# Performance work log

Measured on AMD Instinct MI355X. Metric: run time of the kernel, lower is better.

The kernel has to match this reference:

```python
import jax, jax.numpy as jnp
from jax import lax
import numpy as np

N_QUBITS = 4
N_LAYERS = 2


def _apply_gate(state, M, w):
    # state: [B, 2,2,2,2]; M: [2,2] shared or [B,2,2] batched; acts on wire w
    s = jnp.moveaxis(state, w + 1, 1)
    if M.ndim == 3:
        s = jnp.einsum('bij,bj...->bi...', M, s)
    else:
        s = jnp.einsum('ij,bj...->bi...', M, s)
    return jnp.moveaxis(s, 1, w + 1)


def _apply_cnot(state, c, t):
    # c < t always (chain CNOTs). Move control axis to 1; target axis (t+1) unchanged.
    s = jnp.moveaxis(state, c + 1, 1)
    s0 = s[:, 0]
    s1 = jnp.flip(s[:, 1], axis=t)  # target axis after dropping axis1 is t+1-1 = t
    s = jnp.stack([s0, s1], axis=1)
    return jnp.moveaxis(s, 1, c + 1)


def _quantum_head(q_input, qparams):
    # q_input: [B, n_qubits] rotation angles; qparams: [n_layers, n_qubits, 3]
    B = q_input.shape[0]
    state = jnp.zeros((B, 2 ** N_QUBITS), jnp.complex64).at[:, 0].set(1.0)
    state = state.reshape((B,) + (2,) * N_QUBITS)
    # RY feature map (batched matrices)
    for i in range(N_QUBITS):
        th = q_input[:, i]
        c, s = jnp.cos(th / 2), jnp.sin(th / 2)
        M = jnp.stack([jnp.stack([c, -s], -1), jnp.stack([s, c], -1)], -2)  # [B,2,2]
        state = _apply_gate(state, M.astype(jnp.complex64), i)
    # variational layers
    for layer in range(N_LAYERS):
        for i in range(N_QUBITS):
            phi = qparams[layer, i, 0]
            th = qparams[layer, i, 1]
            om = qparams[layer, i, 2]
            c, s = jnp.cos(th / 2), jnp.sin(th / 2)
            hs, hd = 0.5 * (phi + om), 0.5 * (phi - om)
            M = jnp.stack([
                jnp.stack([jnp.exp(-1j * hs) * c, -jnp.exp(1j * hd) * s]),
                jnp.stack([jnp.exp(-1j * hd) * s, jnp.exp(1j * hs) * c]),
            ])  # [2,2] shared across batch (Rot = RZ(om) RY(th) RZ(phi))
            state = _apply_gate(state, M.astype(jnp.complex64), i)
        for i in range(N_QUBITS - 1):
            state = _apply_cnot(state, i, i + 1)
    # <Z_0> = P(q0=0) - P(q0=1)
    probs = state.real ** 2 + state.imag ** 2
    probs = probs.reshape(B, 2, -1)
    return probs[:, 0].sum(-1) - probs[:, 1].sum(-1)


def _maxpool21(x):
    return lax.reduce_window(x, -np.inf, lax.max, (1, 1, 2, 2), (1, 1, 1, 1), 'VALID')


def setup_inputs() -> dict:
    key = jax.random.key(0)
    ks = jax.random.split(key, 8)
    r = lambda k, s, sc: jax.random.normal(k, s, jnp.float32) * sc
    return {
        'inputs': jax.random.normal(ks[0], (128, 3, 250, 250), jnp.float32),
        'conv1_w': r(ks[1], (6, 3, 5, 5), 0.1),
        'conv1_b': jnp.zeros((6,), jnp.float32),
        'conv2_w': r(ks[2], (15, 6, 3, 3), 0.1),
        'conv2_b': jnp.zeros((15,), jnp.float32),
        'fc1_w': r(ks[3], (120, 55815), 0.004),
        'fc1_b': jnp.zeros((120,), jnp.float32),
        'fc2_w': r(ks[4], (84, 120), 0.09),
        'fc2_b': jnp.zeros((84,), jnp.float32),
        'fc3_w': r(ks[5], (1, 84), 0.1),
        'fc3_b': jnp.zeros((1,), jnp.float32),
        'qparams': jax.random.normal(ks[6], (N_LAYERS, N_QUBITS, 3), jnp.float32),
    }


def reference(inputs, conv1_w, conv1_b, conv2_w, conv2_b, fc1_w, fc1_b,
              fc2_w, fc2_b, fc3_w, fc3_b, qparams):
    dn = ('NCHW', 'OIHW', 'NCHW')
    x = lax.conv_general_dilated(inputs, conv1_w, (2, 2), [(1, 1), (1, 1)],
                                 dimension_numbers=dn) + conv1_b[None, :, None, None]
    x = _maxpool21(jax.nn.relu(x))          # [B,6,123,123]
    x = lax.conv_general_dilated(x, conv2_w, (2, 2), [(1, 1), (1, 1)],
                                 dimension_numbers=dn) + conv2_b[None, :, None, None]
    x = _maxpool21(jax.nn.relu(x))          # [B,15,61,61]
    x = x.reshape(x.shape[0], -1)           # [B,55815]
    x = jax.nn.relu(x @ fc1_w.T + fc1_b)
    x = jax.nn.relu(x @ fc2_w.T + fc2_b)
    x = (x @ fc3_w.T + fc3_b)[:, 0]         # [B]
    q_input = jnp.repeat(x[:, None], N_QUBITS, axis=1)
    q_out = _quantum_head(q_input, qparams)  # [B]
    probs = 0.5 * (q_out + 1.0)
    return jnp.stack([probs, 1.0 - probs], axis=-1)
```

## Files before the change

kernel.cpp:

```cpp
#include <hip/hip_runtime.h>

#define SPLITK 256
#define FC1_K 55815
#define KP 55816

__device__ __forceinline__ unsigned short f2bf(float f) {
    unsigned u = __float_as_uint(f);
    return (unsigned short)((u + 0x7FFFu + ((u >> 16) & 1u)) >> 16);
}

__global__ __launch_bounds__(256) void conv1f_k(const float* __restrict__ in,
                                                const float* __restrict__ w,
                                                const float* __restrict__ bias,
                                                float* __restrict__ out) {
    __shared__ float sbuf[4608];
    const int tc = blockIdx.x, tr = blockIdx.y, b = blockIdx.z;
    const int pr0 = tr * 31, pc0 = tc * 31;
    const int tid = threadIdx.x;
    const int i = tid >> 4, j = tid & 15;
    const int wv = tid >> 6;
    const float* inb = in + (size_t)b * 187500;
    const int ir0 = 2 * pr0 - 1, ic0 = 2 * pc0 - 1;

    {
        int y = tid / 68, x = tid - y * 68;
        #pragma unroll
        for (int it = 0; it < 18; ++it) {
            int gr = ir0 + y, gc = ic0 + x;
            if (!((unsigned)gr < 250u && (unsigned)gc < 250u))
                sbuf[tid + it * 256] = 0.0f;
            x += 52; y += 3;
            if (x >= 68) { x -= 68; ++y; }
        }
    }

    float acc[6][2][2];
    #pragma unroll
    for (int o = 0; o < 6; ++o) {
        float bv = bias[o];
        acc[o][0][0] = bv; acc[o][0][1] = bv; acc[o][1][0] = bv; acc[o][1][1] = bv;
    }

    auto compute_ch = [&](int c) {
        #pragma unroll
        for (int wr = 0; wr < 7; ++wr) {
            const float* rp = &sbuf[(4 * i + wr) * 68 + 4 * j];
            float row[7];
            float4 v4 = *(const float4*)rp;
            float2 v2 = *(const float2*)(rp + 4);
            row[0] = v4.x; row[1] = v4.y; row[2] = v4.z; row[3] = v4.w;
            row[4] = v2.x; row[5] = v2.y; row[6] = rp[6];
            #pragma unroll
            for (int o = 0; o < 6; ++o) {
                #pragma unroll
                for (int kw = 0; kw < 5; ++kw) {
                    if (wr <= 4) {
                        float wv_ = w[o * 75 + c * 25 + wr * 5 + kw];
                        acc[o][0][0] = fmaf(row[kw], wv_, acc[o][0][0]);
                        acc[o][0][1] = fmaf(row[kw + 2], wv_, acc[o][0][1]);
                    }
                    if (wr >= 2) {
                        float wv_ = w[o * 75 + c * 25 + (wr - 2) * 5 + kw];
                        acc[o][1][0] = fmaf(row[kw], wv_, acc[o][1][0]);
                        acc[o][1][1] = fmaf(row[kw + 2], wv_, acc[o][1][1]);
                    }
                }
            }
        }
    };

    for (int c = 0; c < 3; ++c) {
        __syncthreads();
        const float* cp = inb + c * 62500;
        {
            int y = tid / 68, x = tid - y * 68;
            #pragma unroll
            for (int it = 0; it < 18; ++it) {
                int gr = ir0 + y, gc = ic0 + x;
                if ((unsigned)gr < 250u && (unsigned)gc < 250u) {
                    const float* gp = cp + gr * 250 + gc;
                    __builtin_amdgcn_global_load_lds(
                        (const __attribute__((address_space(1))) void*)gp,
                        (__attribute__((address_space(3))) void*)&sbuf[it * 256 + wv * 64],
                        4, 0, 0);
                }
                x += 52; y += 3;
                if (x >= 68) { x -= 68; ++y; }
            }
        }
        __syncthreads();
        compute_ch(c);
    }
    __syncthreads();

    const int gr0 = pr0 + 2 * i, gc0 = pc0 + 2 * j;
    const bool r1in = (2 * i + 1 < 31) && (gr0 + 1 < 123);
    const bool c1in = (2 * j + 1 < 31) && (gc0 + 1 < 123);
    const bool r0in = gr0 < 123, c0in = gc0 < 123;
    #pragma unroll
    for (int g = 0; g < 2; ++g) {
        #pragma unroll
        for (int oo = 0; oo < 3; ++oo)
            #pragma unroll
            for (int di = 0; di < 2; ++di)
                #pragma unroll
                for (int dj = 0; dj < 2; ++dj)
                    sbuf[(oo * 32 + 2 * i + di) * 33 + (2 * j + dj)] =
                        fmaxf(acc[g * 3 + oo][di][dj], 0.0f);
        __syncthreads();
        #pragma unroll
        for (int oo = 0; oo < 3; ++oo) {
            int o = g * 3 + oo;
            const float* p0 = &sbuf[(oo * 32 + 2 * i) * 33 + 2 * j];
            float c00 = p0[0],  c01 = p0[1],  c02 = p0[2];
            float c10 = p0[33], c11 = p0[34], c12 = p0[35];
            float c20 = p0[66], c21 = p0[67], c22 = p0[68];
            float* orow = out + ((size_t)(b * 6 + o) * 123 + gr0) * 123 + gc0;
            if (r0in && c0in) orow[0]   = fmaxf(fmaxf(c00, c01), fmaxf(c10, c11));
            if (r0in && c1in) orow[1]   = fmaxf(fmaxf(c01, c02), fmaxf(c11, c12));
            if (r1in && c0in) orow[123] = fmaxf(fmaxf(c10, c11), fmaxf(c20, c21));
            if (r1in && c1in) orow[124] = fmaxf(fmaxf(c11, c12), fmaxf(c21, c22));
        }
        __syncthreads();
    }
}

__global__ __launch_bounds__(256) void conv2f_k(const float* __restrict__ in,
                                                const float* __restrict__ w,
                                                const float* __restrict__ bias,
                                                unsigned short* __restrict__ out) {
    __shared__ float smem[2000];
    const int tc = blockIdx.x, tr = blockIdx.y, b = blockIdx.z;
    const int pr0 = tr * 15, pc0 = tc * 15;
    const int tid = threadIdx.x;
    const int wv = tid >> 6, lane = tid & 63;
    const int ti = tid >> 4, tj = tid & 15;
    const int tl = ti & 3;
    float* wreg = smem + wv * 320;
    float* halo = smem + 1280;
    const float* inb = in + (size_t)b * 6 * 15129;
    const int irw = 2 * pr0 - 1 + 8 * wv;
    const int ic0 = 2 * pc0 - 1;
    const bool safe = (tr >= 1 && tr <= 3) && (tc >= 1 && tc <= 3);

    int off[5];
    unsigned msk = 0u;
    {
        int y = (lane >= 34) ? 1 : 0;
        int x = lane - 34 * y;
        #pragma unroll
        for (int it = 0; it < 5; ++it) {
            int gr = irw + y, gc = ic0 + x;
            bool valid = ((unsigned)gr < 123u) && ((unsigned)gc < 123u);
            off[it] = valid ? (gr * 123 + gc) : 0;
            msk |= (valid ? 1u : 0u) << it;
            x += 30; ++y;
            if (x >= 34) { x -= 34; ++y; }
        }
    }

    float acc[15];
    #pragma unroll
    for (int o = 0; o < 15; ++o) acc[o] = bias[o];

    for (int c = 0; c < 6; ++c) {
        const float* cp = inb + c * 15129;
        if (safe) {
            #pragma unroll
            for (int it = 0; it < 5; ++it) wreg[lane + it * 64] = cp[off[it]];
        } else {
            #pragma unroll
            for (int it = 0; it < 5; ++it) {
                float v = 0.0f;
                if ((msk >> it) & 1u) v = cp[off[it]];
                wreg[lane + it * 64] = v;
            }
        }
        #pragma unroll
        for (int kh = 0; kh < 3; ++kh) {
            const float* r = &wreg[(2 * tl + kh) * 34 + 2 * tj];
            float a0 = r[0], a1 = r[1], a2 = r[2];
            #pragma unroll
            for (int o = 0; o < 15; ++o) {
                const float* wr_ = &w[o * 54 + c * 9 + kh * 3];
                acc[o] = fmaf(a0, wr_[0], acc[o]);
                acc[o] = fmaf(a1, wr_[1], acc[o]);
                acc[o] = fmaf(a2, wr_[2], acc[o]);
            }
        }
    }

    if (tl == 0 && wv > 0) {
        #pragma unroll
        for (int o = 0; o < 15; ++o)
            halo[(wv - 1) * 240 + o * 16 + tj] = acc[o];
    }
    __syncthreads();

    const int gr = pr0 + ti, gc = pc0 + tj;
    const bool valid = (ti < 15) && (tj < 15) && (gr < 61) && (gc < 61);
    const bool lastrow = (tl == 3);
    const int hb = (wv < 2 ? wv : 2) * 240;
    #pragma unroll
    for (int o = 0; o < 15; ++o) {
        float c00 = acc[o];
        float c01 = __shfl(acc[o], lane + 1);
        float s10 = __shfl(acc[o], lane + 16);
        float s11 = __shfl(acc[o], lane + 17);
        float h10 = halo[hb + o * 16 + tj];
        float h11 = halo[hb + o * 16 + (tj + 1 > 15 ? 15 : tj + 1)];
        float c10 = lastrow ? h10 : s10;
        float c11 = lastrow ? h11 : s11;
        float m = fmaxf(fmaxf(fmaxf(c00, c01), fmaxf(c10, c11)), 0.0f);
        if (valid) out[(size_t)b * KP + o * 3721 + gr * 61 + gc] = f2bf(m);
    }
}

__global__ __launch_bounds__(256) void wcvt_k(const float* __restrict__ W,
                                              unsigned short* __restrict__ Wb) {
    const int n = blockIdx.y;
    const float* src = W + (size_t)n * FC1_K;
    unsigned int* dst = (unsigned int*)(Wb + (size_t)n * KP);
    int base = blockIdx.x * 2048 + threadIdx.x * 2;
    #pragma unroll
    for (int p = 0; p < 4; ++p) {
        int k2 = base + p * 512;
        if (k2 < FC1_K) {
            float v0 = src[k2];
            float v1 = (k2 + 1 < FC1_K) ? src[k2 + 1] : 0.0f;
            dst[k2 >> 1] = (unsigned)f2bf(v0) | ((unsigned)f2bf(v1) << 16);
        }
    }
}

__global__ __launch_bounds__(256) void fc1_k(const unsigned short* __restrict__ Xb,
                                             const unsigned short* __restrict__ Wb,
                                             float* __restrict__ P) {
    using short8 = __attribute__((ext_vector_type(8))) short;
    using f32x4 = __attribute__((ext_vector_type(4))) float;
    __shared__ unsigned short Xs[2][128][40];
    __shared__ unsigned short Ws[2][128][40];
    const int s = blockIdx.x;
    const int ks = s * 224;
    const int ke = min(ks + 224, FC1_K);
    const int tid = threadIdx.x;
    const int row = tid >> 1, cb = (tid & 1) * 16;
    const int wv = tid >> 6, lane = tid & 63;
    const int kb = lane >> 4, lr = lane & 15;

    f32x4 acc[2][8];
    #pragma unroll
    for (int mt = 0; mt < 2; ++mt)
        #pragma unroll
        for (int nt = 0; nt < 8; ++nt)
            acc[mt][nt] = (f32x4){0.f, 0.f, 0.f, 0.f};

    const int nsteps = (ke > ks) ? ((ke - ks + 31) >> 5) : 0;

    auto stage = [&](int buf, int st) {
        const int k0 = ks + st * 32;
        const int krem = ke - k0;
        const unsigned short* xsrc = Xb + (size_t)row * KP + k0 + cb;
        #pragma unroll
        for (int q = 0; q < 2; ++q) {
            int g = cb + q * 8;
            if (g + 8 <= krem) {
                *(uint4*)&Xs[buf][row][g] = *(const uint4*)(xsrc + q * 8);
            } else {
                #pragma unroll
                for (int jj = 0; jj < 8; ++jj)
                    Xs[buf][row][g + jj] = (g + jj < krem) ? xsrc[q * 8 + jj] : (unsigned short)0;
            }
        }
        if (row < 120) {
            const unsigned short* wsrc = Wb + (size_t)row * KP + k0 + cb;
            #pragma unroll
            for (int q = 0; q < 2; ++q) {
                int g = cb + q * 8;
                if (g + 8 <= krem) {
                    *(uint4*)&Ws[buf][row][g] = *(const uint4*)(wsrc + q * 8);
                } else {
                    #pragma unroll
                    for (int jj = 0; jj < 8; ++jj)
                        Ws[buf][row][g + jj] = (g + jj < krem) ? wsrc[q * 8 + jj] : (unsigned short)0;
                }
            }
        } else {
            uint4 z = {0u, 0u, 0u, 0u};
            *(uint4*)&Ws[buf][row][cb] = z;
            *(uint4*)&Ws[buf][row][cb + 8] = z;
        }
    };

    if (nsteps > 0) stage(0, 0);
    int cur = 0;
    for (int st = 0; st < nsteps; ++st) {
        __syncthreads();
        if (st + 1 < nsteps) stage(cur ^ 1, st + 1);
        short8 afr[2];
        #pragma unroll
        for (int mt = 0; mt < 2; ++mt)
            afr[mt] = *(const short8*)&Xs[cur][(wv * 2 + mt) * 16 + lr][kb * 8];
        #pragma unroll
        for (int nt = 0; nt < 8; ++nt) {
            short8 bfr = *(const short8*)&Ws[cur][nt * 16 + lr][kb * 8];
            #pragma unroll
            for (int mt = 0; mt < 2; ++mt)
                acc[mt][nt] = __builtin_amdgcn_mfma_f32_16x16x32_bf16(afr[mt], bfr, acc[mt][nt], 0, 0, 0);
        }
        cur ^= 1;
    }

    float* Pp = P + (size_t)s * 15360;
    #pragma unroll
    for (int mt = 0; mt < 2; ++mt)
        #pragma unroll
        for (int nt = 0; nt < 8; ++nt)
            #pragma unroll
            for (int r = 0; r < 4; ++r) {
                int m = (wv * 2 + mt) * 16 + kb * 4 + r;
                int n = nt * 16 + lr;
                if (n < 120) Pp[m * 120 + n] = acc[mt][nt][r];
            }
}

__global__ __launch_bounds__(512) void tail_k(const float* __restrict__ P,
                                              const float* __restrict__ f1b,
                                              const float* __restrict__ f2w,
                                              const float* __restrict__ f2b,
                                              const float* __restrict__ f3w,
                                              const float* __restrict__ f3b,
                                              const float* __restrict__ qp,
                                              float* __restrict__ out) {
    __shared__ float red[4][120];
    __shared__ float x1[120];
    __shared__ float x2[84];
    int b = blockIdx.x, tid = threadIdx.x;
    if (tid < 480) {
        int part = tid / 120;
        int n = tid - part * 120;
        const float* p = P + (size_t)b * 120 + n;
        float acc = 0.0f;
        #pragma unroll 8
        for (int s = part; s < SPLITK; s += 4)
            acc += p[(size_t)s * 15360];
        red[part][n] = acc;
    }
    __syncthreads();
    if (tid < 120)
        x1[tid] = fmaxf((red[0][tid] + red[1][tid]) + (red[2][tid] + red[3][tid]) + f1b[tid], 0.0f);
    __syncthreads();
    if (tid < 84) {
        float acc = f2b[tid];
        const float* wr = f2w + tid * 120;
        #pragma unroll 4
        for (int n = 0; n < 120; ++n) acc = fmaf(x1[n], wr[n], acc);
        x2[tid] = fmaxf(acc, 0.0f);
    }
    __syncthreads();
    if (tid == 0) {
        float x = f3b[0];
        for (int m = 0; m < 84; ++m) x = fmaf(x2[m], f3w[m], x);
        float sr[16], si[16];
        #pragma unroll
        for (int i = 0; i < 16; ++i) { sr[i] = 0.0f; si[i] = 0.0f; }
        sr[0] = 1.0f;
        float c0 = cosf(0.5f * x), s0 = sinf(0.5f * x);
        #pragma unroll
        for (int w = 0; w < 4; ++w) {
            int mask = 8 >> w;
            #pragma unroll
            for (int idx = 0; idx < 16; ++idx) {
                if (idx & mask) continue;
                int i1 = idx | mask;
                float a0r = sr[idx], a0i = si[idx], a1r = sr[i1], a1i = si[i1];
                sr[idx] = c0 * a0r - s0 * a1r;  si[idx] = c0 * a0i - s0 * a1i;
                sr[i1]  = s0 * a0r + c0 * a1r;  si[i1]  = s0 * a0i + c0 * a1i;
            }
        }
        for (int layer = 0; layer < 2; ++layer) {
            #pragma unroll
            for (int w = 0; w < 4; ++w) {
                int gi = (layer * 4 + w) * 3;
                float phi = qp[gi], th = qp[gi + 1], om = qp[gi + 2];
                float hs = 0.5f * (phi + om), hd = 0.5f * (phi - om);
                float ct = cosf(0.5f * th), st = sinf(0.5f * th);
                float chs = cosf(hs), shs = sinf(hs);
                float chd = cosf(hd), shd = sinf(hd);
                float m00r = chs * ct,  m00i = -shs * ct;
                float m01r = -chd * st, m01i = -shd * st;
                float m10r = chd * st,  m10i = -shd * st;
                float m11r = chs * ct,  m11i = shs * ct;
                int mask = 8 >> w;
                #pragma unroll
                for (int idx = 0; idx < 16; ++idx) {
                    if (idx & mask) continue;
                    int i1 = idx | mask;
                    float a0r = sr[idx], a0i = si[idx], a1r = sr[i1], a1i = si[i1];
                    sr[idx] = m00r * a0r - m00i * a0i + m01r * a1r - m01i * a1i;
                    si[idx] = m00r * a0i + m00i * a0r + m01r * a1i + m01i * a1r;
                    sr[i1]  = m10r * a0r - m10i * a0i + m11r * a1r - m11i * a1i;
                    si[i1]  = m10r * a0i + m10i * a0r + m11r * a1i + m11i * a1r;
                }
            }
            #pragma unroll
            for (int cw = 0; cw < 3; ++cw) {
                int cm = 8 >> cw, tm = 8 >> (cw + 1);
                #pragma unroll
                for (int idx = 0; idx < 16; ++idx) {
                    if ((idx & cm) && !(idx & tm)) {
                        int i1 = idx | tm;
                        float tr = sr[idx]; sr[idx] = sr[i1]; sr[i1] = tr;
                        float ti = si[idx]; si[idx] = si[i1]; si[i1] = ti;
                    }
                }
            }
        }
        float q = 0.0f;
        #pragma unroll
        for (int idx = 0; idx < 16; ++idx) {
            float p2 = sr[idx] * sr[idx] + si[idx] * si[idx];
            q += (idx < 8) ? p2 : -p2;
        }
        float pr = 0.5f * (q + 1.0f);
        out[2 * b] = pr;
        out[2 * b + 1] = 1.0f - pr;
    }
}

extern "C" void kernel_launch(void* const* d_in, const int* in_sizes, int n_in,
                              void* d_out, int out_size, void* d_ws, size_t ws_size,
                              hipStream_t stream) {
    const float* inp = (const float*)d_in[0];
    const float* c1w = (const float*)d_in[1];
    const float* c1b = (const float*)d_in[2];
    const float* c2w = (const float*)d_in[3];
    const float* c2b = (const float*)d_in[4];
    const float* f1w = (const float*)d_in[5];
    const float* f1b = (const float*)d_in[6];
    const float* f2w = (const float*)d_in[7];
    const float* f2b = (const float*)d_in[8];
    const float* f3w = (const float*)d_in[9];
    const float* f3b = (const float*)d_in[10];
    const float* qp  = (const float*)d_in[11];
    float* out = (float*)d_out;
    float* ws = (float*)d_ws;

    float* B = ws;
    unsigned short* Db = (unsigned short*)(ws + 11619072);
    float* P = ws + 15191296;
    unsigned short* Wb = (unsigned short*)(ws + 19123456);

    wcvt_k<<<dim3(28, 120), 256, 0, stream>>>(f1w, Wb);
    conv1f_k<<<dim3(4, 4, 128), 256, 0, stream>>>(inp, c1w, c1b, B);
    conv2f_k<<<dim3(5, 5, 128), 256, 0, stream>>>(B, c2w, c2b, Db);
    fc1_k<<<dim3(SPLITK), 256, 0, stream>>>(Db, Wb, P);
    tail_k<<<128, 512, 0, stream>>>(P, f1b, f2w, f2b, f3w, f3b, qp, out);
}
```

Before: 145.0 us.

## Restructure conv1 into per-wave row tiles with shuffle-based maxpool

The conv1+relu+maxpool kernel moves from 31x31 pooled tiles with 2x2 outputs per thread to 15x15 tiles with one conv output per thread. Each wave stages its own 10x36 input window in LDS via regular loads, which removes the block-wide barriers around the staging. The 2x2 stride-1 maxpool now uses wavefront shuffles plus a small LDS halo between waves instead of a full LDS round trip. The grid grows from 4x4 to 9x9 tiles per image, trading more redundant halo loads and less register reuse for higher occupancy and fewer synchronisations.

Measured after the change: 205.6 us. 1.42x slower.

```diff
diff --git a/kernel.cpp b/kernel.cpp
--- a/kernel.cpp
+++ b/kernel.cpp
@@ -13,115 +13,100 @@
                                                 const float* __restrict__ w,
                                                 const float* __restrict__ bias,
                                                 float* __restrict__ out) {
-    __shared__ float sbuf[4608];
+    __shared__ float smem[1872];
     const int tc = blockIdx.x, tr = blockIdx.y, b = blockIdx.z;
-    const int pr0 = tr * 31, pc0 = tc * 31;
+    const int pr0 = tr * 15, pc0 = tc * 15;
     const int tid = threadIdx.x;
-    const int i = tid >> 4, j = tid & 15;
-    const int wv = tid >> 6;
+    const int wv = tid >> 6, lane = tid & 63;
+    const int ti = tid >> 4, tj = tid & 15;
+    const int tl = ti & 3;
+    float* wreg = smem + wv * 396;
+    float* halo = smem + 1584;
     const float* inb = in + (size_t)b * 187500;
-    const int ir0 = 2 * pr0 - 1, ic0 = 2 * pc0 - 1;
-
+    const int irw = 2 * pr0 - 1 + 8 * wv;
+    const int ic0 = 2 * pc0 - 1;
+    const bool safe = (tr >= 1 && tr <= 7) && (tc >= 1 && tc <= 7);
+
+    int off[7];
+    unsigned msk = 0u;
     {
-        int y = tid / 68, x = tid - y * 68;
-        #pragma unroll
-        for (int it = 0; it < 18; ++it) {
-            int gr = ir0 + y, gc = ic0 + x;
-            if (!((unsigned)gr < 250u && (unsigned)gc < 250u))
-                sbuf[tid + it * 256] = 0.0f;
-            x += 52; y += 3;
-            if (x >= 68) { x -= 68; ++y; }
-        }
-    }
-
-    float acc[6][2][2];
+        int y = lane / 36;
+        int x = lane - y * 36;
+        #pragma unroll
+        for (int it = 0; it < 7; ++it) {
+            int gr = irw + y, gc = ic0 + x;
+            bool valid = ((unsigned)gr < 250u) && ((unsigned)gc < 250u) && (it < 6 || lane < 12);
+            off[it] = valid ? (gr * 250 + gc) : 0;
+            msk |= (valid ? 1u : 0u) << it;
+            x += 28; ++y;
+            if (x >= 36) { x -= 36; ++y; }
+        }
+    }
+
+    float acc[6];
+    #pragma unroll
+    for (int o = 0; o < 6; ++o) acc[o] = bias[o];
+
+    for (int c = 0; c < 3; ++c) {
+        const float* cp = inb + c * 62500;
+        if (safe) {
+            #pragma unroll
+            for (int it = 0; it < 6; ++it) wreg[lane + it * 64] = cp[off[it]];
+            if (lane < 12) wreg[384 + lane] = cp[off[6]];
+        } else {
+            #pragma unroll
+            for (int it = 0; it < 6; ++it) {
+                float v = 0.0f;
+                if ((msk >> it) & 1u) v = cp[off[it]];
+                wreg[lane + it * 64] = v;
+            }
+            if (lane < 12) {
+                float v = 0.0f;
+                if ((msk >> 6) & 1u) v = cp[off[6]];
+                wreg[384 + lane] = v;
+            }
+        }
+        #pragma unroll
+        for (int kh = 0; kh < 5; ++kh) {
+            const float* rp = &wreg[(2 * tl + kh) * 36 + 2 * tj];
+            float r0, r1, r2, r3, r4;
+            float4 v4 = *(const float4*)rp;
+            r0 = v4.x; r1 = v4.y; r2 = v4.z; r3 = v4.w; r4 = rp[4];
+            #pragma unroll
+            for (int o = 0; o < 6; ++o) {
+                const float* wr_ = &w[o * 75 + c * 25 + kh * 5];
+                acc[o] = fmaf(r0, wr_[0], acc[o]);
+                acc[o] = fmaf(r1, wr_[1], acc[o]);
+                acc[o] = fmaf(r2, wr_[2], acc[o]);
+                acc[o] = fmaf(r3, wr_[3], acc[o]);
+                acc[o] = fmaf(r4, wr_[4], acc[o]);
+            }
+        }
+    }
+
+    if (tl == 0 && wv > 0) {
+        #pragma unroll
+        for (int o = 0; o < 6; ++o)
+            halo[(wv - 1) * 96 + o * 16 + tj] = acc[o];
+    }
+    __syncthreads();
+
+    const int gr = pr0 + ti, gc = pc0 + tj;
+    const bool valid = (ti < 15) && (tj < 15) && (gr < 123) && (gc < 123);
+    const bool lastrow = (tl == 3);
+    const int hb = (wv < 2 ? wv : 2) * 96;
     #pragma unroll
     for (int o = 0; o < 6; ++o) {
-        float bv = bias[o];
-        acc[o][0][0] = bv; acc[o][0][1] = bv; acc[o][1][0] = bv; acc[o][1][1] = bv;
-    }
-
-    auto compute_ch = [&](int c) {
-        #pragma unroll
-        for (int wr = 0; wr < 7; ++wr) {
-            const float* rp = &sbuf[(4 * i + wr) * 68 + 4 * j];
-            float row[7];
-            float4 v4 = *(const float4*)rp;
-            float2 v2 = *(const float2*)(rp + 4);
-            row[0] = v4.x; row[1] = v4.y; row[2] = v4.z; row[3] = v4.w;
-            row[4] = v2.x; row[5] = v2.y; row[6] = rp[6];
-            #pragma unroll
-            for (int o = 0; o < 6; ++o) {
-                #pragma unroll
-                for (int kw = 0; kw < 5; ++kw) {
-                    if (wr <= 4) {
-                        float wv_ = w[o * 75 + c * 25 + wr * 5 + kw];
-                        acc[o][0][0] = fmaf(row[kw], wv_, acc[o][0][0]);
-                        acc[o][0][1] = fmaf(row[kw + 2], wv_, acc[o][0][1]);
-                    }
-                    if (wr >= 2) {
-                        float wv_ = w[o * 75 + c * 25 + (wr - 2) * 5 + kw];
-                        acc[o][1][0] = fmaf(row[kw], wv_, acc[o][1][0]);
-                        acc[o][1][1] = fmaf(row[kw + 2], wv_, acc[o][1][1]);
-                    }
-                }
-            }
-        }
-    };
-
-    for (int c = 0; c < 3; ++c) {
-        __syncthreads();
-        const float* cp = inb + c * 62500;
-        {
-            int y = tid / 68, x = tid - y * 68;
-            #pragma unroll
-            for (int it = 0; it < 18; ++it) {
-                int gr = ir0 + y, gc = ic0 + x;
-                if ((unsigned)gr < 250u && (unsigned)gc < 250u) {
-                    const float* gp = cp + gr * 250 + gc;
-                    __builtin_amdgcn_global_load_lds(
-                        (const __attribute__((address_space(1))) void*)gp,
-                        (__attribute__((address_space(3))) void*)&sbuf[it * 256 + wv * 64],
-                        4, 0, 0);
-                }
-                x += 52; y += 3;
-                if (x >= 68) { x -= 68; ++y; }
-            }
-        }
-        __syncthreads();
-        compute_ch(c);
-    }
-    __syncthreads();
-
-    const int gr0 = pr0 + 2 * i, gc0 = pc0 + 2 * j;
-    const bool r1in = (2 * i + 1 < 31) && (gr0 + 1 < 123);
-    const bool c1in = (2 * j + 1 < 31) && (gc0 + 1 < 123);
-    const bool r0in = gr0 < 123, c0in = gc0 < 123;
-    #pragma unroll
-    for (int g = 0; g < 2; ++g) {
-        #pragma unroll
-        for (int oo = 0; oo < 3; ++oo)
-            #pragma unroll
-            for (int di = 0; di < 2; ++di)
-                #pragma unroll
-                for (int dj = 0; dj < 2; ++dj)
-                    sbuf[(oo * 32 + 2 * i + di) * 33 + (2 * j + dj)] =
-                        fmaxf(acc[g * 3 + oo][di][dj], 0.0f);
-        __syncthreads();
-        #pragma unroll
-        for (int oo = 0; oo < 3; ++oo) {
-            int o = g * 3 + oo;
-            const float* p0 = &sbuf[(oo * 32 + 2 * i) * 33 + 2 * j];
-            float c00 = p0[0],  c01 = p0[1],  c02 = p0[2];
-            float c10 = p0[33], c11 = p0[34], c12 = p0[35];
-            float c20 = p0[66], c21 = p0[67], c22 = p0[68];
-            float* orow = out + ((size_t)(b * 6 + o) * 123 + gr0) * 123 + gc0;
-            if (r0in && c0in) orow[0]   = fmaxf(fmaxf(c00, c01), fmaxf(c10, c11));
-            if (r0in && c1in) orow[1]   = fmaxf(fmaxf(c01, c02), fmaxf(c11, c12));
-            if (r1in && c0in) orow[123] = fmaxf(fmaxf(c10, c11), fmaxf(c20, c21));
-            if (r1in && c1in) orow[124] = fmaxf(fmaxf(c11, c12), fmaxf(c21, c22));
-        }
-        __syncthreads();
+        float c00 = acc[o];
+        float c01 = __shfl(acc[o], lane + 1);
+        float s10 = __shfl(acc[o], lane + 16);
+        float s11 = __shfl(acc[o], lane + 17);
+        float h10 = halo[hb + o * 16 + tj];
+        float h11 = halo[hb + o * 16 + (tj + 1 > 15 ? 15 : tj + 1)];
+        float c10 = lastrow ? h10 : s10;
+        float c11 = lastrow ? h11 : s11;
+        float m = fmaxf(fmaxf(fmaxf(c00, c01), fmaxf(c10, c11)), 0.0f);
+        if (valid) out[((size_t)(b * 6 + o) * 123 + gr) * 123 + gc] = m;
     }
 }
 
@@ -452,7 +437,7 @@
     unsigned short* Wb = (unsigned short*)(ws + 19123456);
 
     wcvt_k<<<dim3(28, 120), 256, 0, stream>>>(f1w, Wb);
-    conv1f_k<<<dim3(4, 4, 128), 256, 0, stream>>>(inp, c1w, c1b, B);
+    conv1f_k<<<dim3(9, 9, 128), 256, 0, stream>>>(inp, c1w, c1b, B);
     conv2f_k<<<dim3(5, 5, 128), 256, 0, stream>>>(B, c2w, c2b, Db);
     fc1_k<<<dim3(SPLITK), 256, 0, stream>>>(Db, Wb, P);
     tail_k<<<128, 512, 0, stream>>>(P, f1b, f2w, f2b, f3w, f3b, qp, out);
```
